# Kernel tuning notes

Measured on AMD Instinct MI355X. Metric: run time of the kernel, lower is better.

Reference implementation:

```python
import jax, jax.numpy as jnp
import numpy as np

NUM_SCENES = 7
SHAPE = [512, 512, 256, 64]  # layer dims: 512->512->256->64
BATCH = 16384


def _xavier(key, shape):
    # nn.init.xavier_normal_ on (s, in, out): fan_in/fan_out from last two dims
    fan_in, fan_out = shape[-2], shape[-1]
    std = np.sqrt(2.0 / (fan_in + fan_out)).astype(np.float32)
    return jax.random.normal(key, shape, dtype=jnp.float32) * std


def setup_inputs() -> dict:
    key = jax.random.key(0)
    ks = jax.random.split(key, 16)
    inp = {
        "x": jax.random.normal(ks[0], (BATCH, SHAPE[0]), dtype=jnp.float32),
        "scene": jax.random.randint(ks[1], (BATCH,), 1, NUM_SCENES + 1, dtype=jnp.int64),
    }
    for i in range(3):
        din, dout = SHAPE[i], SHAPE[i + 1]
        inp[f"W{i}"] = _xavier(ks[2 + 4 * i], (NUM_SCENES, din, dout))
        inp[f"b{i}"] = jnp.zeros((NUM_SCENES, dout), dtype=jnp.float32)
        inp[f"gW{i}"] = _xavier(ks[3 + 4 * i], (1, din, dout))
        inp[f"gb{i}"] = jnp.zeros((1, dout), dtype=jnp.float32)
    return inp


def _star_linear(x, scene0, W, b, gW, gb, relu):
    # W: (S, in, out), gW: (1, in, out). Equivalent to gathering W[scene0]
    # and doing x[:,None,:] @ (w * gW), but computed as a dense GEMM over
    # all scenes followed by a per-sample select (avoids B*in*out gather).
    scaled = W * gW                                   # (S, in, out)
    out_all = jnp.einsum('bi,sio->bso', x, scaled)    # (B, S, out)
    out = jnp.take_along_axis(out_all, scene0[:, None, None], axis=1)[:, 0, :]
    out = out + b[scene0] + gb[0]
    if relu:
        out = jnp.maximum(out, 0.0)
    return out  # dropout is identity at eval


def reference(x, scene, W0, b0, gW0, gb0, W1, b1, gW1, gb1, W2, b2, gW2, gb2):
    scene0 = (scene - 1).astype(jnp.int32)
    h = _star_linear(x, scene0, W0, b0, gW0, gb0, relu=True)
    h = _star_linear(h, scene0, W1, b1, gW1, gb1, relu=True)
    h = _star_linear(h, scene0, W2, b2, gW2, gb2, relu=False)  # drop=True -> no relu
    return h
```

## Files before the change

### kernel.cpp

```cpp
#include <hip/hip_runtime.h>
#include <hip/hip_bf16.h>
#include <stdint.h>


#define BATCH   16384
#define NSCENE  7
#define TM      128
#define NBLK    (BATCH / 256)
#define MT_MAX  (BATCH / TM + NSCENE)
#define PADMAX  (BATCH + NSCENE * TM)

typedef __bf16 bf16x8 __attribute__((ext_vector_type(8)));
typedef float  f32x4  __attribute__((ext_vector_type(4)));

__device__ __forceinline__ ushort f2bf(float f) {
  union { float f; uint32_t u; } v; v.f = f;
  uint32_t r = (v.u + 0x7FFFu + ((v.u >> 16) & 1u)) >> 16;
  return (ushort)r;
}
__device__ __forceinline__ uint32_t pk2(float a, float b) {
  union { __hip_bfloat162 h; uint32_t u; } cv;
  cv.h = __float22bfloat162_rn(float2{a, b});
  return cv.u;
}
__device__ __forceinline__ void async16(const void* g, void* lds) {
  __builtin_amdgcn_global_load_lds(
      (const __attribute__((address_space(1))) uint32_t*)g,
      (__attribute__((address_space(3))) uint32_t*)lds, 16, 0, 0);
}

__device__ __forceinline__ void st_tile(const float* __restrict__ W,
                                        const float* __restrict__ gW,
                                        ushort* __restrict__ sT,
                                        int K, int N, int s, int n0, int k0,
                                        int tid) {
  __shared__ float tl[32][33];
  int tx = tid & 31, ty = tid >> 5;
  const float* Wp = W + (size_t)s * K * N;
#pragma unroll
  for (int i = 0; i < 4; i++) {
    int k = k0 + ty + i * 8;
    tl[ty + i * 8][tx] = Wp[(size_t)k * N + n0 + tx] * gW[(size_t)k * N + n0 + tx];
  }
  __syncthreads();
#pragma unroll
  for (int i = 0; i < 4; i++) {
    int n = n0 + ty + i * 8;
    sT[((size_t)s * N + n) * K + k0 + tx] = f2bf(tl[tx][ty + i * 8]);
  }
}

#define NB_W0 (16 * 16 * 7)
#define NB_W1 (8 * 16 * 7)
#define NB_W2 (2 * 8 * 7)
#define NB_BIAS 23
#define NB_CNT NBLK

__global__ __launch_bounds__(256) void prep_k(
    const float* __restrict__ W0, const float* __restrict__ gW0,
    const float* __restrict__ W1, const float* __restrict__ gW1,
    const float* __restrict__ W2, const float* __restrict__ gW2,
    const float* __restrict__ b0, const float* __restrict__ gb0,
    const float* __restrict__ b1, const float* __restrict__ gb1,
    const float* __restrict__ b2, const float* __restrict__ gb2,
    const int* __restrict__ scene,
    ushort* __restrict__ sT0, ushort* __restrict__ sT1, ushort* __restrict__ sT2,
    float* __restrict__ bias0, float* __restrict__ bias1, float* __restrict__ bias2,
    int* __restrict__ bcnt) {
  int bid = blockIdx.x, tid = threadIdx.x;
  if (bid < NB_W0) {
    int l = bid;
    st_tile(W0, gW0, sT0, 512, 512, l / 256, (l % 16) * 32, ((l / 16) % 16) * 32, tid);
  } else if (bid < NB_W0 + NB_W1) {
    int l = bid - NB_W0;
    st_tile(W1, gW1, sT1, 512, 256, l / 128, (l % 8) * 32, ((l / 8) % 16) * 32, tid);
  } else if (bid < NB_W0 + NB_W1 + NB_W2) {
    int l = bid - NB_W0 - NB_W1;
    st_tile(W2, gW2, sT2, 256, 64, l / 16, (l % 2) * 32, ((l / 2) % 8) * 32, tid);
  } else if (bid < NB_W0 + NB_W1 + NB_W2 + NB_BIAS) {
    int t = (bid - NB_W0 - NB_W1 - NB_W2) * 256 + tid;
    if (t < 7 * 512) bias0[t] = b0[t] + gb0[t & 511];
    else if (t < 7 * 512 + 7 * 256) { int i = t - 7 * 512; bias1[i] = b1[i] + gb1[i & 255]; }
    else if (t < 7 * 512 + 7 * 256 + 7 * 64) { int i = t - 7 * 512 - 7 * 256; bias2[i] = b2[i] + gb2[i & 63]; }
  } else {
    __shared__ int l[NSCENE];
    if (tid < NSCENE) l[tid] = 0;
    __syncthreads();
    int blk = bid - NB_W0 - NB_W1 - NB_W2 - NB_BIAS;
    atomicAdd(&l[scene[blk * 256 + tid] - 1], 1);
    __syncthreads();
    if (tid < NSCENE) bcnt[blk * NSCENE + tid] = l[tid];
  }
}

__global__ void plan_k(const int* __restrict__ bcnt, int* __restrict__ meta,
                       int* __restrict__ bbase, int* __restrict__ idxp) {
  __shared__ int tot[NSCENE], pstart[NSCENE], pend[NSCENE];
  int tid = threadIdx.x;
  if (tid < NSCENE) {
    int c = 0;
    for (int b = 0; b < NBLK; b++) c += bcnt[b * NSCENE + tid];
    tot[tid] = c;
  }
  __syncthreads();
  if (tid == 0) {
    int po = 0, t = 0;
    for (int s = 0; s < NSCENE; s++) {
      meta[16 + s] = po;
      int tiles = (tot[s] + TM - 1) / TM;
      pstart[s] = po + tot[s];
      pend[s] = po + tiles * TM;
      for (int j = 0; j < tiles; j++) { meta[32 + t] = s; meta[192 + t] = po + j * TM; t++; }
      po += tiles * TM;
    }
    meta[24] = t;
  }
  __syncthreads();
  if (tid < NSCENE) {
    int run = meta[16 + tid];
    for (int b = 0; b < NBLK; b++) { bbase[b * NSCENE + tid] = run; run += bcnt[b * NSCENE + tid]; }
  }
  for (int s = 0; s < NSCENE; s++)
    for (int i = pstart[s] + tid; i < pend[s]; i += 256) idxp[i] = -1;
}

__global__ void scatter_k(const int* __restrict__ scene,
                          const int* __restrict__ bbase, int* __restrict__ idxp) {
  __shared__ int l[NSCENE];
  if (threadIdx.x < NSCENE) l[threadIdx.x] = 0;
  __syncthreads();
  int i = blockIdx.x * 256 + threadIdx.x;
  int s = scene[i] - 1;
  int pos = atomicAdd(&l[s], 1);
  idxp[bbase[blockIdx.x * NSCENE + s] + pos] = i;
}

template<int KDIM, int NDIM, int TN, bool GATHER_A, bool RELU, bool SCATTER_OUT>
__global__ __launch_bounds__(256) void gemm_k(
    const float* __restrict__ xin, const ushort* __restrict__ ain,
    const ushort* __restrict__ bw, const float* __restrict__ bias,
    const int* __restrict__ meta, const int* __restrict__ idxp,
    ushort* __restrict__ hout, float* __restrict__ out) {
  int t = blockIdx.x;
  if (t >= meta[24]) return;
  int sc = meta[32 + t];
  int mrow0 = meta[192 + t];
  int nb = blockIdx.y;

  constexpr int WN = TN / 2;
  constexpr int ACCN = WN / 16;

  __shared__ __align__(16) ushort Abuf[TM * 64];
  __shared__ __align__(16) ushort Bbuf[TN * 64];

  int tid = threadIdx.x;
  int lane = tid & 63, wid = tid >> 6;
  int wm = wid >> 1, wn = wid & 1;

  f32x4 acc[4][ACCN];
#pragma unroll
  for (int mt = 0; mt < 4; mt++)
#pragma unroll
    for (int nt = 0; nt < ACCN; nt++) acc[mt][nt] = (f32x4){0.f, 0.f, 0.f, 0.f};

  int idxc[4];
  if (GATHER_A) {
#pragma unroll
    for (int i = 0; i < 4; i++) idxc[i] = idxp[mrow0 + (tid >> 3) + i * 32];
  }

  const ushort* bwS = bw + ((size_t)sc * NDIM + (size_t)nb * TN) * KDIM;

  for (int kb = 0; kb < KDIM / 64; kb++) {
    if (GATHER_A) {
#pragma unroll
      for (int i = 0; i < 4; i++) {
        int c = tid + i * 256;
        int row = c >> 3, q = c & 7;
        int kg = q ^ (row & 7);
        uint4 val;
        int g = idxc[i];
        if (g >= 0) {
          const float4* p = (const float4*)(xin + (size_t)g * 512 + kb * 64 + kg * 8);
          float4 f0 = p[0], f1 = p[1];
          val.x = pk2(f0.x, f0.y); val.y = pk2(f0.z, f0.w);
          val.z = pk2(f1.x, f1.y); val.w = pk2(f1.z, f1.w);
        } else {
          val = make_uint4(0, 0, 0, 0);
        }
        *(uint4*)(&Abuf[c * 8]) = val;
      }
    } else {
#pragma unroll
      for (int i = 0; i < 4; i++) {
        int c = tid + i * 256;
        int row = c >> 3, q = c & 7;
        int kg = q ^ (row & 7);
        async16(ain + (size_t)(mrow0 + row) * KDIM + kb * 64 + kg * 8,
                &Abuf[(size_t)(i * 256 + wid * 64) * 8]);
      }
    }
#pragma unroll
    for (int i = 0; i < TN * 8 / 256; i++) {
      int c = tid + i * 256;
      int row = c >> 3, q = c & 7;
      int kg = q ^ (row & 7);
      async16(bwS + (size_t)row * KDIM + kb * 64 + kg * 8,
              &Bbuf[(size_t)(i * 256 + wid * 64) * 8]);
    }
    __syncthreads();
#pragma unroll
    for (int kk = 0; kk < 64; kk += 32) {
      bf16x8 af[4], bfr[ACCN];
      int kc = (kk >> 3) + (lane >> 4);
#pragma unroll
      for (int mt = 0; mt < 4; mt++) {
        int row = wm * 64 + mt * 16 + (lane & 15);
        af[mt] = *(const bf16x8*)(&Abuf[(row * 8 + (kc ^ (row & 7))) * 8]);
      }
#pragma unroll
      for (int nt = 0; nt < ACCN; nt++) {
        int row = wn * WN + nt * 16 + (lane & 15);
        bfr[nt] = *(const bf16x8*)(&Bbuf[(row * 8 + (kc ^ (row & 7))) * 8]);
      }
#pragma unroll
      for (int mt = 0; mt < 4; mt++)
#pragma unroll
        for (int nt = 0; nt < ACCN; nt++)
          acc[mt][nt] = __builtin_amdgcn_mfma_f32_16x16x32_bf16(af[mt], bfr[nt], acc[mt][nt], 0, 0, 0);
    }
    __syncthreads();
  }

  int gidx[4][4];
  if (SCATTER_OUT) {
#pragma unroll
    for (int mt = 0; mt < 4; mt++)
#pragma unroll
      for (int r = 0; r < 4; r++)
        gidx[mt][r] = idxp[mrow0 + wm * 64 + mt * 16 + (lane >> 4) * 4 + r];
  }
#pragma unroll
  for (int mt = 0; mt < 4; mt++) {
    int rl0 = wm * 64 + mt * 16 + (lane >> 4) * 4;
#pragma unroll
    for (int nt = 0; nt < ACCN; nt++) {
      int col = nb * TN + wn * WN + nt * 16 + (lane & 15);
      float bv = bias[sc * NDIM + col];
#pragma unroll
      for (int r = 0; r < 4; r++) {
        float v = acc[mt][nt][r] + bv;
        if (RELU) v = fmaxf(v, 0.f);
        if (SCATTER_OUT) {
          int g = gidx[mt][r];
          if (g >= 0) out[(size_t)g * NDIM + col] = v;
        } else {
          hout[(size_t)(mrow0 + rl0 + r) * NDIM + col] = f2bf(v);
        }
      }
    }
  }
}

extern "C" void kernel_launch(void* const* d_in, const int* in_sizes, int n_in,
                              void* d_out, int out_size, void* d_ws, size_t ws_size,
                              hipStream_t stream) {
  const float* x   = (const float*)d_in[0];
  const int* scene = (const int*)d_in[1];
  const float* W0  = (const float*)d_in[2];
  const float* b0  = (const float*)d_in[3];
  const float* gW0 = (const float*)d_in[4];
  const float* gb0 = (const float*)d_in[5];
  const float* W1  = (const float*)d_in[6];
  const float* b1  = (const float*)d_in[7];
  const float* gW1 = (const float*)d_in[8];
  const float* gb1 = (const float*)d_in[9];
  const float* W2  = (const float*)d_in[10];
  const float* b2  = (const float*)d_in[11];
  const float* gW2 = (const float*)d_in[12];
  const float* gb2 = (const float*)d_in[13];
  float* out = (float*)d_out;

  char* ws = (char*)d_ws;
  size_t off = 0;
  auto alloc = [&](size_t bytes) -> void* {
    void* p = ws + off;
    off = (off + bytes + 255) & ~(size_t)255;
    return p;
  };
  ushort* sT0   = (ushort*)alloc((size_t)7 * 512 * 512 * 2);
  ushort* sT1   = (ushort*)alloc((size_t)7 * 256 * 512 * 2);
  ushort* sT2   = (ushort*)alloc((size_t)7 * 64 * 256 * 2);
  float*  bias0 = (float*)alloc(7 * 512 * 4);
  float*  bias1 = (float*)alloc(7 * 256 * 4);
  float*  bias2 = (float*)alloc(7 * 64 * 4);
  int*    meta  = (int*)alloc(1024 * 4);
  int*    bcnt  = (int*)alloc(NBLK * NSCENE * 4);
  int*    bbase = (int*)alloc(NBLK * NSCENE * 4);
  int*    idxp  = (int*)alloc(PADMAX * 4);
  ushort* hc1   = (ushort*)alloc((size_t)PADMAX * 512 * 2);
  ushort* hc2   = (ushort*)alloc((size_t)PADMAX * 256 * 2);
  (void)ws_size; (void)n_in; (void)in_sizes; (void)out_size;

  prep_k<<<NB_W0 + NB_W1 + NB_W2 + NB_BIAS + NB_CNT, 256, 0, stream>>>(
      W0, gW0, W1, gW1, W2, gW2, b0, gb0, b1, gb1, b2, gb2, scene,
      sT0, sT1, sT2, bias0, bias1, bias2, bcnt);
  plan_k<<<1, 256, 0, stream>>>(bcnt, meta, bbase, idxp);
  scatter_k<<<NBLK, 256, 0, stream>>>(scene, bbase, idxp);

  gemm_k<512, 512, 128, true,  true,  false><<<dim3(MT_MAX, 4), 256, 0, stream>>>(
      x, nullptr, sT0, bias0, meta, idxp, hc1, nullptr);
  gemm_k<512, 256, 128, false, true,  false><<<dim3(MT_MAX, 2), 256, 0, stream>>>(
      nullptr, hc1, sT1, bias1, meta, idxp, hc2, nullptr);
  gemm_k<256, 64, 64,  false, false, true ><<<dim3(MT_MAX, 1), 256, 0, stream>>>(
      nullptr, hc2, sT2, bias2, meta, idxp, nullptr, out);
}
```

Measured before the change: 166.7 us.

## Fuse all stages into one persistent kernel with software grid barriers

Replaces the six separate launches (prep, plan, scatter, three GEMMs) with a single persistent kernel whose blocks loop over work items, separated by atomic-counter grid barriers. The first-layer input gather is split into an explicit pass that writes a compacted bf16 copy of x in scene order, so the first GEMM can use async LDS loads. The aim is to remove launch gaps and tail effects between stages. In exchange it pays for grid-wide spin barriers and an extra round trip of the converted input through memory. It also relies on every block being co-resident, since the grid is sized from occupancy with a normal launch rather than a cooperative one.

```diff
diff --git a/kernel.cpp b/kernel.cpp
--- a/kernel.cpp
+++ b/kernel.cpp
@@ -7,7 +7,6 @@
 #define NSCENE  7
 #define TM      128
 #define NBLK    (BATCH / 256)
-#define MT_MAX  (BATCH / TM + NSCENE)
 #define PADMAX  (BATCH + NSCENE * TM)
 
 typedef __bf16 bf16x8 __attribute__((ext_vector_type(8)));
@@ -20,7 +19,7 @@
 }
 __device__ __forceinline__ uint32_t pk2(float a, float b) {
   union { __hip_bfloat162 h; uint32_t u; } cv;
-  cv.h = __float22bfloat162_rn(float2{a, b});
+  cv.h = __float22bfloat162_rn(make_float2(a, b));
   return cv.u;
 }
 __device__ __forceinline__ void async16(const void* g, void* lds) {
@@ -29,237 +28,261 @@
       (__attribute__((address_space(3))) uint32_t*)lds, 16, 0, 0);
 }
 
-__device__ __forceinline__ void st_tile(const float* __restrict__ W,
-                                        const float* __restrict__ gW,
-                                        ushort* __restrict__ sT,
-                                        int K, int N, int s, int n0, int k0,
-                                        int tid) {
-  __shared__ float tl[32][33];
-  int tx = tid & 31, ty = tid >> 5;
-  const float* Wp = W + (size_t)s * K * N;
-#pragma unroll
-  for (int i = 0; i < 4; i++) {
-    int k = k0 + ty + i * 8;
-    tl[ty + i * 8][tx] = Wp[(size_t)k * N + n0 + tx] * gW[(size_t)k * N + n0 + tx];
-  }
+__device__ __forceinline__ void gsync(int* bar, int G, int gen) {
   __syncthreads();
-#pragma unroll
-  for (int i = 0; i < 4; i++) {
-    int n = n0 + ty + i * 8;
-    sT[((size_t)s * N + n) * K + k0 + tx] = f2bf(tl[tx][ty + i * 8]);
-  }
+  __threadfence();
+  if (threadIdx.x == 0) {
+    __hip_atomic_fetch_add(bar, 1, __ATOMIC_ACQ_REL, __HIP_MEMORY_SCOPE_AGENT);
+    while (__hip_atomic_load(bar, __ATOMIC_ACQUIRE, __HIP_MEMORY_SCOPE_AGENT) < G * gen)
+      __builtin_amdgcn_s_sleep(2);
+  }
+  __syncthreads();
+  __threadfence();
 }
 
 #define NB_W0 (16 * 16 * 7)
 #define NB_W1 (8 * 16 * 7)
 #define NB_W2 (2 * 8 * 7)
 #define NB_BIAS 23
-#define NB_CNT NBLK
-
-__global__ __launch_bounds__(256) void prep_k(
+#define NB_PREP (NB_W0 + NB_W1 + NB_W2 + NB_BIAS + NBLK)
+
+__device__ __forceinline__ void st_tile(const float* __restrict__ W,
+                                        const float* __restrict__ gW,
+                                        ushort* __restrict__ sT,
+                                        float (*tl)[33],
+                                        int K, int N, int s, int n0, int k0,
+                                        int tid) {
+  int tx = tid & 31, ty = tid >> 5;
+  const float* Wp = W + (size_t)s * K * N;
+#pragma unroll
+  for (int i = 0; i < 4; i++) {
+    int k = k0 + ty + i * 8;
+    tl[ty + i * 8][tx] = Wp[(size_t)k * N + n0 + tx] * gW[(size_t)k * N + n0 + tx];
+  }
+  __syncthreads();
+#pragma unroll
+  for (int i = 0; i < 4; i++) {
+    int n = n0 + ty + i * 8;
+    sT[((size_t)s * N + n) * K + k0 + tx] = f2bf(tl[tx][ty + i * 8]);
+  }
+  __syncthreads();
+}
+
+template<int KDIM, int NDIM, int TN, int NBJ, bool RELU, bool SCATTER_OUT>
+__device__ __forceinline__ void gemm_phase(
+    const ushort* __restrict__ ain, const ushort* __restrict__ bw,
+    const float* __restrict__ bias, const int* __restrict__ meta,
+    const int* __restrict__ idxp, ushort* __restrict__ hout,
+    float* __restrict__ out, ushort* Abuf, ushort* Bbuf,
+    int ntiles, int G, int bid, int tid) {
+  constexpr int WN = TN / 2;
+  constexpr int ACCN = WN / 16;
+  int lane = tid & 63, wid = tid >> 6;
+  int wm = wid >> 1, wn = wid & 1;
+
+  for (int j = bid; j < ntiles * NBJ; j += G) {
+    int t = j / NBJ, nb = j % NBJ;
+    int sc = meta[32 + t];
+    int mrow0 = meta[192 + t];
+
+    f32x4 acc[4][ACCN];
+#pragma unroll
+    for (int mt = 0; mt < 4; mt++)
+#pragma unroll
+      for (int nt = 0; nt < ACCN; nt++) acc[mt][nt] = (f32x4){0.f, 0.f, 0.f, 0.f};
+
+    const ushort* bwS = bw + ((size_t)sc * NDIM + (size_t)nb * TN) * KDIM;
+
+    for (int kb = 0; kb < KDIM / 64; kb++) {
+#pragma unroll
+      for (int i = 0; i < 4; i++) {
+        int c = tid + i * 256;
+        int row = c >> 3, q = c & 7;
+        int kg = q ^ (row & 7);
+        async16(ain + (size_t)(mrow0 + row) * KDIM + kb * 64 + kg * 8,
+                &Abuf[(size_t)(i * 256 + wid * 64) * 8]);
+      }
+#pragma unroll
+      for (int i = 0; i < TN * 8 / 256; i++) {
+        int c = tid + i * 256;
+        int row = c >> 3, q = c & 7;
+        int kg = q ^ (row & 7);
+        async16(bwS + (size_t)row * KDIM + kb * 64 + kg * 8,
+                &Bbuf[(size_t)(i * 256 + wid * 64) * 8]);
+      }
+      __syncthreads();
+#pragma unroll
+      for (int kk = 0; kk < 64; kk += 32) {
+        bf16x8 af[4], bfr[ACCN];
+        int kc = (kk >> 3) + (lane >> 4);
+#pragma unroll
+        for (int mt = 0; mt < 4; mt++) {
+          int row = wm * 64 + mt * 16 + (lane & 15);
+          af[mt] = *(const bf16x8*)(&Abuf[(row * 8 + (kc ^ (row & 7))) * 8]);
+        }
+#pragma unroll
+        for (int nt = 0; nt < ACCN; nt++) {
+          int row = wn * WN + nt * 16 + (lane & 15);
+          bfr[nt] = *(const bf16x8*)(&Bbuf[(row * 8 + (kc ^ (row & 7))) * 8]);
+        }
+#pragma unroll
+        for (int mt = 0; mt < 4; mt++)
+#pragma unroll
+          for (int nt = 0; nt < ACCN; nt++)
+            acc[mt][nt] = __builtin_amdgcn_mfma_f32_16x16x32_bf16(af[mt], bfr[nt], acc[mt][nt], 0, 0, 0);
+      }
+      __syncthreads();
+    }
+
+    int gidx[4][4];
+    if (SCATTER_OUT) {
+#pragma unroll
+      for (int mt = 0; mt < 4; mt++)
+#pragma unroll
+        for (int r = 0; r < 4; r++)
+          gidx[mt][r] = idxp[mrow0 + wm * 64 + mt * 16 + (lane >> 4) * 4 + r];
+    }
+#pragma unroll
+    for (int mt = 0; mt < 4; mt++) {
+      int rl0 = wm * 64 + mt * 16 + (lane >> 4) * 4;
+#pragma unroll
+      for (int nt = 0; nt < ACCN; nt++) {
+        int col = nb * TN + wn * WN + nt * 16 + (lane & 15);
+        float bv = bias[sc * NDIM + col];
+#pragma unroll
+        for (int r = 0; r < 4; r++) {
+          float v = acc[mt][nt][r] + bv;
+          if (RELU) v = fmaxf(v, 0.f);
+          if (SCATTER_OUT) {
+            int g = gidx[mt][r];
+            if (g >= 0) out[(size_t)g * NDIM + col] = v;
+          } else {
+            hout[(size_t)(mrow0 + rl0 + r) * NDIM + col] = f2bf(v);
+          }
+        }
+      }
+    }
+  }
+}
+
+__global__ void init_k(int* bar) { if (threadIdx.x == 0) *bar = 0; }
+
+__global__ __launch_bounds__(256, 2) void mega_k(
+    const float* __restrict__ x, const int* __restrict__ scene,
     const float* __restrict__ W0, const float* __restrict__ gW0,
     const float* __restrict__ W1, const float* __restrict__ gW1,
     const float* __restrict__ W2, const float* __restrict__ gW2,
     const float* __restrict__ b0, const float* __restrict__ gb0,
     const float* __restrict__ b1, const float* __restrict__ gb1,
     const float* __restrict__ b2, const float* __restrict__ gb2,
-    const int* __restrict__ scene,
     ushort* __restrict__ sT0, ushort* __restrict__ sT1, ushort* __restrict__ sT2,
     float* __restrict__ bias0, float* __restrict__ bias1, float* __restrict__ bias2,
-    int* __restrict__ bcnt) {
-  int bid = blockIdx.x, tid = threadIdx.x;
-  if (bid < NB_W0) {
-    int l = bid;
-    st_tile(W0, gW0, sT0, 512, 512, l / 256, (l % 16) * 32, ((l / 16) % 16) * 32, tid);
-  } else if (bid < NB_W0 + NB_W1) {
-    int l = bid - NB_W0;
-    st_tile(W1, gW1, sT1, 512, 256, l / 128, (l % 8) * 32, ((l / 8) % 16) * 32, tid);
-  } else if (bid < NB_W0 + NB_W1 + NB_W2) {
-    int l = bid - NB_W0 - NB_W1;
-    st_tile(W2, gW2, sT2, 256, 64, l / 16, (l % 2) * 32, ((l / 2) % 8) * 32, tid);
-  } else if (bid < NB_W0 + NB_W1 + NB_W2 + NB_BIAS) {
-    int t = (bid - NB_W0 - NB_W1 - NB_W2) * 256 + tid;
-    if (t < 7 * 512) bias0[t] = b0[t] + gb0[t & 511];
-    else if (t < 7 * 512 + 7 * 256) { int i = t - 7 * 512; bias1[i] = b1[i] + gb1[i & 255]; }
-    else if (t < 7 * 512 + 7 * 256 + 7 * 64) { int i = t - 7 * 512 - 7 * 256; bias2[i] = b2[i] + gb2[i & 63]; }
-  } else {
-    __shared__ int l[NSCENE];
-    if (tid < NSCENE) l[tid] = 0;
+    int* __restrict__ bcnt, int* __restrict__ bbase, int* __restrict__ meta,
+    int* __restrict__ idxp, int* __restrict__ destg, ushort* __restrict__ xc,
+    ushort* __restrict__ hc1, ushort* __restrict__ hc2,
+    float* __restrict__ out, int* bar) {
+  __shared__ __align__(16) ushort Abuf[TM * 64];
+  __shared__ __align__(16) ushort Bbuf[TM * 64];
+  __shared__ float tl[32][33];
+  __shared__ int shl[NSCENE];
+  __shared__ int sdest[256];
+
+  int G = gridDim.x, bid = blockIdx.x, tid = threadIdx.x;
+
+  for (int j = bid; j < NB_PREP; j += G) {
+    if (j < NB_W0) {
+      st_tile(W0, gW0, sT0, tl, 512, 512, j / 256, (j % 16) * 32, ((j / 16) % 16) * 32, tid);
+    } else if (j < NB_W0 + NB_W1) {
+      int l = j - NB_W0;
+      st_tile(W1, gW1, sT1, tl, 512, 256, l / 128, (l % 8) * 32, ((l / 8) % 16) * 32, tid);
+    } else if (j < NB_W0 + NB_W1 + NB_W2) {
+      int l = j - NB_W0 - NB_W1;
+      st_tile(W2, gW2, sT2, tl, 256, 64, l / 16, (l % 2) * 32, ((l / 2) % 8) * 32, tid);
+    } else if (j < NB_W0 + NB_W1 + NB_W2 + NB_BIAS) {
+      int t = (j - NB_W0 - NB_W1 - NB_W2) * 256 + tid;
+      if (t < 7 * 512) bias0[t] = b0[t] + gb0[t & 511];
+      else if (t < 7 * 512 + 7 * 256) { int i = t - 7 * 512; bias1[i] = b1[i] + gb1[i & 255]; }
+      else if (t < 7 * 512 + 7 * 256 + 7 * 64) { int i = t - 7 * 512 - 7 * 256; bias2[i] = b2[i] + gb2[i & 63]; }
+    } else {
+      int blk = j - NB_W0 - NB_W1 - NB_W2 - NB_BIAS;
+      if (tid < NSCENE) shl[tid] = 0;
+      __syncthreads();
+      atomicAdd(&shl[scene[blk * 256 + tid] - 1], 1);
+      __syncthreads();
+      if (tid < NSCENE) bcnt[blk * NSCENE + tid] = shl[tid];
+      __syncthreads();
+    }
+  }
+  gsync(bar, G, 1);
+
+  if (bid == 0) {
+    __shared__ int tot[NSCENE], pstart[NSCENE], pend[NSCENE];
+    if (tid < NSCENE) {
+      int c = 0;
+      for (int b = 0; b < NBLK; b++) c += bcnt[b * NSCENE + tid];
+      tot[tid] = c;
+    }
     __syncthreads();
-    int blk = bid - NB_W0 - NB_W1 - NB_W2 - NB_BIAS;
-    atomicAdd(&l[scene[blk * 256 + tid] - 1], 1);
+    if (tid == 0) {
+      int po = 0, t = 0;
+      for (int s = 0; s < NSCENE; s++) {
+        meta[16 + s] = po;
+        int tiles = (tot[s] + TM - 1) / TM;
+        pstart[s] = po + tot[s];
+        pend[s] = po + tiles * TM;
+        for (int jj = 0; jj < tiles; jj++) { meta[32 + t] = s; meta[192 + t] = po + jj * TM; t++; }
+        po += tiles * TM;
+      }
+      meta[24] = t;
+    }
     __syncthreads();
-    if (tid < NSCENE) bcnt[blk * NSCENE + tid] = l[tid];
-  }
-}
-
-__global__ void plan_k(const int* __restrict__ bcnt, int* __restrict__ meta,
-                       int* __restrict__ bbase, int* __restrict__ idxp) {
-  __shared__ int tot[NSCENE], pstart[NSCENE], pend[NSCENE];
-  int tid = threadIdx.x;
-  if (tid < NSCENE) {
-    int c = 0;
-    for (int b = 0; b < NBLK; b++) c += bcnt[b * NSCENE + tid];
-    tot[tid] = c;
-  }
-  __syncthreads();
-  if (tid == 0) {
-    int po = 0, t = 0;
-    for (int s = 0; s < NSCENE; s++) {
-      meta[16 + s] = po;
-      int tiles = (tot[s] + TM - 1) / TM;
-      pstart[s] = po + tot[s];
-      pend[s] = po + tiles * TM;
-      for (int j = 0; j < tiles; j++) { meta[32 + t] = s; meta[192 + t] = po + j * TM; t++; }
-      po += tiles * TM;
-    }
-    meta[24] = t;
-  }
-  __syncthreads();
-  if (tid < NSCENE) {
-    int run = meta[16 + tid];
-    for (int b = 0; b < NBLK; b++) { bbase[b * NSCENE + tid] = run; run += bcnt[b * NSCENE + tid]; }
-  }
-  for (int s = 0; s < NSCENE; s++)
-    for (int i = pstart[s] + tid; i < pend[s]; i += 256) idxp[i] = -1;
-}
-
-__global__ void scatter_k(const int* __restrict__ scene,
-                          const int* __restrict__ bbase, int* __restrict__ idxp) {
-  __shared__ int l[NSCENE];
-  if (threadIdx.x < NSCENE) l[threadIdx.x] = 0;
-  __syncthreads();
-  int i = blockIdx.x * 256 + threadIdx.x;
-  int s = scene[i] - 1;
-  int pos = atomicAdd(&l[s], 1);
-  idxp[bbase[blockIdx.x * NSCENE + s] + pos] = i;
-}
-
-template<int KDIM, int NDIM, int TN, bool GATHER_A, bool RELU, bool SCATTER_OUT>
-__global__ __launch_bounds__(256) void gemm_k(
-    const float* __restrict__ xin, const ushort* __restrict__ ain,
-    const ushort* __restrict__ bw, const float* __restrict__ bias,
-    const int* __restrict__ meta, const int* __restrict__ idxp,
-    ushort* __restrict__ hout, float* __restrict__ out) {
-  int t = blockIdx.x;
-  if (t >= meta[24]) return;
-  int sc = meta[32 + t];
-  int mrow0 = meta[192 + t];
-  int nb = blockIdx.y;
-
-  constexpr int WN = TN / 2;
-  constexpr int ACCN = WN / 16;
-
-  __shared__ __align__(16) ushort Abuf[TM * 64];
-  __shared__ __align__(16) ushort Bbuf[TN * 64];
-
-  int tid = threadIdx.x;
-  int lane = tid & 63, wid = tid >> 6;
-  int wm = wid >> 1, wn = wid & 1;
-
-  f32x4 acc[4][ACCN];
-#pragma unroll
-  for (int mt = 0; mt < 4; mt++)
-#pragma unroll
-    for (int nt = 0; nt < ACCN; nt++) acc[mt][nt] = (f32x4){0.f, 0.f, 0.f, 0.f};
-
-  int idxc[4];
-  if (GATHER_A) {
-#pragma unroll
-    for (int i = 0; i < 4; i++) idxc[i] = idxp[mrow0 + (tid >> 3) + i * 32];
-  }
-
-  const ushort* bwS = bw + ((size_t)sc * NDIM + (size_t)nb * TN) * KDIM;
-
-  for (int kb = 0; kb < KDIM / 64; kb++) {
-    if (GATHER_A) {
-#pragma unroll
-      for (int i = 0; i < 4; i++) {
-        int c = tid + i * 256;
-        int row = c >> 3, q = c & 7;
-        int kg = q ^ (row & 7);
-        uint4 val;
-        int g = idxc[i];
-        if (g >= 0) {
-          const float4* p = (const float4*)(xin + (size_t)g * 512 + kb * 64 + kg * 8);
-          float4 f0 = p[0], f1 = p[1];
-          val.x = pk2(f0.x, f0.y); val.y = pk2(f0.z, f0.w);
-          val.z = pk2(f1.x, f1.y); val.w = pk2(f1.z, f1.w);
-        } else {
-          val = make_uint4(0, 0, 0, 0);
-        }
-        *(uint4*)(&Abuf[c * 8]) = val;
-      }
-    } else {
-#pragma unroll
-      for (int i = 0; i < 4; i++) {
-        int c = tid + i * 256;
-        int row = c >> 3, q = c & 7;
-        int kg = q ^ (row & 7);
-        async16(ain + (size_t)(mrow0 + row) * KDIM + kb * 64 + kg * 8,
-                &Abuf[(size_t)(i * 256 + wid * 64) * 8]);
-      }
-    }
-#pragma unroll
-    for (int i = 0; i < TN * 8 / 256; i++) {
-      int c = tid + i * 256;
-      int row = c >> 3, q = c & 7;
-      int kg = q ^ (row & 7);
-      async16(bwS + (size_t)row * KDIM + kb * 64 + kg * 8,
-              &Bbuf[(size_t)(i * 256 + wid * 64) * 8]);
-    }
+    if (tid < NSCENE) {
+      int run = meta[16 + tid];
+      for (int b = 0; b < NBLK; b++) { bbase[b * NSCENE + tid] = run; run += bcnt[b * NSCENE + tid]; }
+    }
+    for (int s = 0; s < NSCENE; s++)
+      for (int i = pstart[s] + tid; i < pend[s]; i += 256) idxp[i] = -1;
+  }
+  gsync(bar, G, 2);
+
+  for (int j = bid; j < NBLK; j += G) {
+    if (tid < NSCENE) shl[tid] = 0;
     __syncthreads();
-#pragma unroll
-    for (int kk = 0; kk < 64; kk += 32) {
-      bf16x8 af[4], bfr[ACCN];
-      int kc = (kk >> 3) + (lane >> 4);
-#pragma unroll
-      for (int mt = 0; mt < 4; mt++) {
-        int row = wm * 64 + mt * 16 + (lane & 15);
-        af[mt] = *(const bf16x8*)(&Abuf[(row * 8 + (kc ^ (row & 7))) * 8]);
-      }
-#pragma unroll
-      for (int nt = 0; nt < ACCN; nt++) {
-        int row = wn * WN + nt * 16 + (lane & 15);
-        bfr[nt] = *(const bf16x8*)(&Bbuf[(row * 8 + (kc ^ (row & 7))) * 8]);
-      }
-#pragma unroll
-      for (int mt = 0; mt < 4; mt++)
-#pragma unroll
-        for (int nt = 0; nt < ACCN; nt++)
-          acc[mt][nt] = __builtin_amdgcn_mfma_f32_16x16x32_bf16(af[mt], bfr[nt], acc[mt][nt], 0, 0, 0);
-    }
+    int i = j * 256 + tid;
+    int s = scene[i] - 1;
+    int pos = atomicAdd(&shl[s], 1);
+    int dest = bbase[j * NSCENE + s] + pos;
+    idxp[dest] = i;
+    destg[i] = dest;
     __syncthreads();
   }
-
-  int gidx[4][4];
-  if (SCATTER_OUT) {
-#pragma unroll
-    for (int mt = 0; mt < 4; mt++)
-#pragma unroll
-      for (int r = 0; r < 4; r++)
-        gidx[mt][r] = idxp[mrow0 + wm * 64 + mt * 16 + (lane >> 4) * 4 + r];
-  }
-#pragma unroll
-  for (int mt = 0; mt < 4; mt++) {
-    int rl0 = wm * 64 + mt * 16 + (lane >> 4) * 4;
-#pragma unroll
-    for (int nt = 0; nt < ACCN; nt++) {
-      int col = nb * TN + wn * WN + nt * 16 + (lane & 15);
-      float bv = bias[sc * NDIM + col];
-#pragma unroll
-      for (int r = 0; r < 4; r++) {
-        float v = acc[mt][nt][r] + bv;
-        if (RELU) v = fmaxf(v, 0.f);
-        if (SCATTER_OUT) {
-          int g = gidx[mt][r];
-          if (g >= 0) out[(size_t)g * NDIM + col] = v;
-        } else {
-          hout[(size_t)(mrow0 + rl0 + r) * NDIM + col] = f2bf(v);
-        }
-      }
-    }
-  }
+  gsync(bar, G, 3);
+
+  for (int j = bid; j < BATCH / 8; j += G) {
+    int base = j * 8;
+    for (int k = tid; k < 512; k += 256) {
+      int r = base + (k >> 6), c = k & 63;
+      int d = destg[r];
+      const float4* p = (const float4*)(x + (size_t)r * 512 + c * 8);
+      float4 f0 = p[0], f1 = p[1];
+      uint4 v;
+      v.x = pk2(f0.x, f0.y); v.y = pk2(f0.z, f0.w);
+      v.z = pk2(f1.x, f1.y); v.w = pk2(f1.z, f1.w);
+      *(uint4*)(xc + (size_t)d * 512 + c * 8) = v;
+    }
+  }
+  gsync(bar, G, 4);
+
+  int ntiles = meta[24];
+
+  gemm_phase<512, 512, 128, 4, true,  false>(xc,  sT0, bias0, meta, idxp, hc1, nullptr,
+                                             Abuf, Bbuf, ntiles, G, bid, tid);
+  gsync(bar, G, 5);
+  gemm_phase<512, 256, 128, 2, true,  false>(hc1, sT1, bias1, meta, idxp, hc2, nullptr,
+                                             Abuf, Bbuf, ntiles, G, bid, tid);
+  gsync(bar, G, 6);
+  gemm_phase<256, 64,  64,  1, false, true >(hc2, sT2, bias2, meta, idxp, nullptr, out,
+                                             Abuf, Bbuf, ntiles, G, bid, tid);
 }
 
 extern "C" void kernel_launch(void* const* d_in, const int* in_sizes, int n_in,
@@ -298,20 +321,23 @@
   int*    bcnt  = (int*)alloc(NBLK * NSCENE * 4);
   int*    bbase = (int*)alloc(NBLK * NSCENE * 4);
   int*    idxp  = (int*)alloc(PADMAX * 4);
+  int*    destg = (int*)alloc(BATCH * 4);
+  ushort* xc    = (ushort*)alloc((size_t)PADMAX * 512 * 2);
   ushort* hc1   = (ushort*)alloc((size_t)PADMAX * 512 * 2);
   ushort* hc2   = (ushort*)alloc((size_t)PADMAX * 256 * 2);
+  int*    bar   = (int*)alloc(256);
   (void)ws_size; (void)n_in; (void)in_sizes; (void)out_size;
 
-  prep_k<<<NB_W0 + NB_W1 + NB_W2 + NB_BIAS + NB_CNT, 256, 0, stream>>>(
-      W0, gW0, W1, gW1, W2, gW2, b0, gb0, b1, gb1, b2, gb2, scene,
-      sT0, sT1, sT2, bias0, bias1, bias2, bcnt);
-  plan_k<<<1, 256, 0, stream>>>(bcnt, meta, bbase, idxp);
-  scatter_k<<<NBLK, 256, 0, stream>>>(scene, bbase, idxp);
-
-  gemm_k<512, 512, 128, true,  true,  false><<<dim3(MT_MAX, 4), 256, 0, stream>>>(
-      x, nullptr, sT0, bias0, meta, idxp, hc1, nullptr);
-  gemm_k<512, 256, 128, false, true,  false><<<dim3(MT_MAX, 2), 256, 0, stream>>>(
-      nullptr, hc1, sT1, bias1, meta, idxp, hc2, nullptr);
-  gemm_k<256, 64, 64,  false, false, true ><<<dim3(MT_MAX, 1), 256, 0, stream>>>(
-      nullptr, hc2, sT2, bias2, meta, idxp, nullptr, out);
-}
+  int occ = 0;
+  (void)hipOccupancyMaxActiveBlocksPerMultiprocessor(&occ, mega_k, 256, 0);
+  if (occ < 1) occ = 1;
+  if (occ > 4) occ = 4;
+  int G = occ * 256;
+
+  init_k<<<1, 64, 0, stream>>>(bar);
+  hipLaunchKernelGGL(mega_k, dim3(G), dim3(256), 0, stream,
+                     x, scene, W0, gW0, W1, gW1, W2, gW2,
+                     b0, gb0, b1, gb1, b2, gb2,
+                     sT0, sT1, sT2, bias0, bias1, bias2,
+                     bcnt, bbase, meta, idxp, destg, xc, hc1, hc2, out, bar);
+}
```

Measured after the change: 547.7 us. 3.29x slower.

## Precompact input to bf16 in a separate kernel and use async loads in layer 0

Applied to the files above, without the earlier changes.

The scatter kernel now also records each sample's destination row. A new kernel converts x to bf16 once and writes it into a scene-compacted, padded buffer. The first GEMM then loads A tiles with async global-to-LDS copies, like the other layers, instead of doing per-row fp32 gathers and bf16 conversion in every N-block. This removes the redundant gather and conversion done by each of the four N-blocks, at the cost of an extra launch and an extra write and read of a 16 MB bf16 buffer. Padding rows of the new buffer are left uninitialised rather than zeroed.

```diff
diff --git a/kernel.cpp b/kernel.cpp
--- a/kernel.cpp
+++ b/kernel.cpp
@@ -20,7 +20,7 @@
 }
 __device__ __forceinline__ uint32_t pk2(float a, float b) {
   union { __hip_bfloat162 h; uint32_t u; } cv;
-  cv.h = __float22bfloat162_rn(float2{a, b});
+  cv.h = __float22bfloat162_rn(make_float2(a, b));
   return cv.u;
 }
 __device__ __forceinline__ void async16(const void* g, void* lds) {
@@ -125,22 +125,42 @@
 }
 
 __global__ void scatter_k(const int* __restrict__ scene,
-                          const int* __restrict__ bbase, int* __restrict__ idxp) {
+                          const int* __restrict__ bbase, int* __restrict__ idxp,
+                          int* __restrict__ destg) {
   __shared__ int l[NSCENE];
   if (threadIdx.x < NSCENE) l[threadIdx.x] = 0;
   __syncthreads();
   int i = blockIdx.x * 256 + threadIdx.x;
   int s = scene[i] - 1;
   int pos = atomicAdd(&l[s], 1);
-  idxp[bbase[blockIdx.x * NSCENE + s] + pos] = i;
-}
-
-template<int KDIM, int NDIM, int TN, bool GATHER_A, bool RELU, bool SCATTER_OUT>
+  int dest = bbase[blockIdx.x * NSCENE + s] + pos;
+  idxp[dest] = i;
+  destg[i] = dest;
+}
+
+__global__ __launch_bounds__(256) void xc_k(const float* __restrict__ x,
+                                            const int* __restrict__ destg,
+                                            ushort* __restrict__ xc) {
+  int r = blockIdx.x * 8 + (threadIdx.x >> 5);
+  int c = (threadIdx.x & 31) * 16;
+  int d = destg[r];
+  const float4* p = (const float4*)(x + (size_t)r * 512 + c);
+  float4 f0 = p[0], f1 = p[1], f2 = p[2], f3 = p[3];
+  uint4 v0, v1;
+  v0.x = pk2(f0.x, f0.y); v0.y = pk2(f0.z, f0.w);
+  v0.z = pk2(f1.x, f1.y); v0.w = pk2(f1.z, f1.w);
+  v1.x = pk2(f2.x, f2.y); v1.y = pk2(f2.z, f2.w);
+  v1.z = pk2(f3.x, f3.y); v1.w = pk2(f3.z, f3.w);
+  uint4* q = (uint4*)(xc + (size_t)d * 512 + c);
+  q[0] = v0; q[1] = v1;
+}
+
+template<int KDIM, int NDIM, int TN, bool RELU, bool SCATTER_OUT>
 __global__ __launch_bounds__(256) void gemm_k(
-    const float* __restrict__ xin, const ushort* __restrict__ ain,
-    const ushort* __restrict__ bw, const float* __restrict__ bias,
-    const int* __restrict__ meta, const int* __restrict__ idxp,
-    ushort* __restrict__ hout, float* __restrict__ out) {
+    const ushort* __restrict__ ain, const ushort* __restrict__ bw,
+    const float* __restrict__ bias, const int* __restrict__ meta,
+    const int* __restrict__ idxp, ushort* __restrict__ hout,
+    float* __restrict__ out) {
   int t = blockIdx.x;
   if (t >= meta[24]) return;
   int sc = meta[32 + t];
@@ -163,42 +183,16 @@
 #pragma unroll
     for (int nt = 0; nt < ACCN; nt++) acc[mt][nt] = (f32x4){0.f, 0.f, 0.f, 0.f};
 
-  int idxc[4];
-  if (GATHER_A) {
-#pragma unroll
-    for (int i = 0; i < 4; i++) idxc[i] = idxp[mrow0 + (tid >> 3) + i * 32];
-  }
-
   const ushort* bwS = bw + ((size_t)sc * NDIM + (size_t)nb * TN) * KDIM;
 
   for (int kb = 0; kb < KDIM / 64; kb++) {
-    if (GATHER_A) {
-#pragma unroll
-      for (int i = 0; i < 4; i++) {
-        int c = tid + i * 256;
-        int row = c >> 3, q = c & 7;
-        int kg = q ^ (row & 7);
-        uint4 val;
-        int g = idxc[i];
-        if (g >= 0) {
-          const float4* p = (const float4*)(xin + (size_t)g * 512 + kb * 64 + kg * 8);
-          float4 f0 = p[0], f1 = p[1];
-          val.x = pk2(f0.x, f0.y); val.y = pk2(f0.z, f0.w);
-          val.z = pk2(f1.x, f1.y); val.w = pk2(f1.z, f1.w);
-        } else {
-          val = make_uint4(0, 0, 0, 0);
-        }
-        *(uint4*)(&Abuf[c * 8]) = val;
-      }
-    } else {
-#pragma unroll
-      for (int i = 0; i < 4; i++) {
-        int c = tid + i * 256;
-        int row = c >> 3, q = c & 7;
-        int kg = q ^ (row & 7);
-        async16(ain + (size_t)(mrow0 + row) * KDIM + kb * 64 + kg * 8,
-                &Abuf[(size_t)(i * 256 + wid * 64) * 8]);
-      }
+#pragma unroll
+    for (int i = 0; i < 4; i++) {
+      int c = tid + i * 256;
+      int row = c >> 3, q = c & 7;
+      int kg = q ^ (row & 7);
+      async16(ain + (size_t)(mrow0 + row) * KDIM + kb * 64 + kg * 8,
+              &Abuf[(size_t)(i * 256 + wid * 64) * 8]);
     }
 #pragma unroll
     for (int i = 0; i < TN * 8 / 256; i++) {
@@ -298,6 +292,8 @@
   int*    bcnt  = (int*)alloc(NBLK * NSCENE * 4);
   int*    bbase = (int*)alloc(NBLK * NSCENE * 4);
   int*    idxp  = (int*)alloc(PADMAX * 4);
+  int*    destg = (int*)alloc(BATCH * 4);
+  ushort* xc    = (ushort*)alloc((size_t)PADMAX * 512 * 2);
   ushort* hc1   = (ushort*)alloc((size_t)PADMAX * 512 * 2);
   ushort* hc2   = (ushort*)alloc((size_t)PADMAX * 256 * 2);
   (void)ws_size; (void)n_in; (void)in_sizes; (void)out_size;
@@ -306,12 +302,13 @@
       W0, gW0, W1, gW1, W2, gW2, b0, gb0, b1, gb1, b2, gb2, scene,
       sT0, sT1, sT2, bias0, bias1, bias2, bcnt);
   plan_k<<<1, 256, 0, stream>>>(bcnt, meta, bbase, idxp);
-  scatter_k<<<NBLK, 256, 0, stream>>>(scene, bbase, idxp);
-
-  gemm_k<512, 512, 128, true,  true,  false><<<dim3(MT_MAX, 4), 256, 0, stream>>>(
-      x, nullptr, sT0, bias0, meta, idxp, hc1, nullptr);
-  gemm_k<512, 256, 128, false, true,  false><<<dim3(MT_MAX, 2), 256, 0, stream>>>(
-      nullptr, hc1, sT1, bias1, meta, idxp, hc2, nullptr);
-  gemm_k<256, 64, 64,  false, false, true ><<<dim3(MT_MAX, 1), 256, 0, stream>>>(
-      nullptr, hc2, sT2, bias2, meta, idxp, nullptr, out);
-}
+  scatter_k<<<NBLK, 256, 0, stream>>>(scene, bbase, idxp, destg);
+  xc_k<<<BATCH / 8, 256, 0, stream>>>(x, destg, xc);
+
+  gemm_k<512, 512, 128, true,  false><<<dim3(MT_MAX, 4), 256, 0, stream>>>(
+      xc, sT0, bias0, meta, idxp, hc1, nullptr);
+  gemm_k<512, 256, 128, true,  false><<<dim3(MT_MAX, 2), 256, 0, stream>>>(
+      hc1, sT1, bias1, meta, idxp, hc2, nullptr);
+  gemm_k<256, 64,  64,  false, true ><<<dim3(MT_MAX, 1), 256, 0, stream>>>(
+      hc2, sT2, bias2, meta, idxp, nullptr, out);
+}
```

Result: slower. 170.1 us (+2.0%).
